# Performance work log

Measured on AMD Instinct MI355X. Metric: run time of the kernel, lower is better.

Reference implementation:

```python
import jax, jax.numpy as jnp
import numpy as np

B, T, F = 16, 2048, 512


def setup_inputs() -> dict:
    key = jax.random.key(0)
    k1, k2, k3 = jax.random.split(key, 3)
    x = jax.random.normal(k1, (B, T, F), dtype=jnp.float32)
    w_aggr = jax.random.normal(k2, (F, 1), dtype=jnp.float32) * 0.02
    b_aggr = jnp.zeros((1,), dtype=jnp.float32)
    # lengths in [T//2, T] to avoid degenerate lengths[0]==0 (torch would div by 0 too)
    seq_len = jax.random.randint(k3, (B,), T // 2, T + 1).astype(jnp.int32)
    return {"x": x, "w_aggr": w_aggr, "b_aggr": b_aggr, "seq_len": seq_len}


def reference(x, w_aggr, b_aggr, seq_len):
    """Valley-detection dynamic segment-mean pooling.

    Faithful to the torch code, but the O(T^2) triangular-mask bmm is
    expressed as the mathematically identical prefix-sum difference:
    bmm(utri[end]-utri[start], v) == cumsum(v)[end] - cumsum(v)[start].
    Output time dim is padded to T (>= dynamic max_counts); padded segment
    rows have start==end==0 -> numerator 0 / clamp -> exactly 0, matching
    the torch zero-padded `valleys` rows.
    """
    Bx, Tx, Fx = x.shape
    wt = jax.nn.sigmoid(x @ w_aggr + b_aggr)[..., 0]          # [B,T] gate weights
    before = jnp.pad(wt[:, :-1], ((0, 0), (1, 0)))            # pad 0 (sigmoid>0 => pos 0 never valley)
    after = jnp.pad(wt[:, 1:], ((0, 0), (0, 1)))              # pad 0 => pos T-1 never valley
    valley = (wt < before) & (wt < after)                     # [B,T] strict local minima
    starts_mask = valley.at[:, 0].set(True)                   # mask[:,0]=True
    ends_mask = valley.at[:, 0].set(False).at[:, -1].set(True)  # mask[:,0]=False; mask[:,-1]=True

    t = jnp.arange(Tx, dtype=jnp.int32)
    bi = jnp.arange(Bx)[:, None]

    def pack(m, vals):
        # left-pack values at True positions into fixed [B,T] (zeros beyond count)
        rank = jnp.cumsum(m, axis=1) - 1
        slot = jnp.where(m, rank, Tx)                         # dump non-selected into slot T
        out = jnp.zeros((Bx, Tx + 1), jnp.int32).at[bi, slot].set(vals)
        return out[:, :Tx], jnp.sum(m, axis=1)

    starts, counts = pack(starts_mask, jnp.broadcast_to(t, (Bx, Tx)))
    end_vals = jnp.broadcast_to(jnp.minimum(t + 2, Tx), (Bx, Tx))  # valley_index_end clipped to length
    ends, _ = pack(ends_mask, end_vals)

    alpha_h = wt[..., None] * x                               # [B,T,F]
    # exclusive->inclusive prefix sums with leading zero row
    cs_ah = jnp.concatenate([jnp.zeros((Bx, 1, Fx), x.dtype), jnp.cumsum(alpha_h, axis=1)], axis=1)
    cs_w = jnp.concatenate([jnp.zeros((Bx, 1), x.dtype), jnp.cumsum(wt, axis=1)], axis=1)

    num = cs_ah[bi, ends] - cs_ah[bi, starts]                 # [B,T,F] segment sums of w*x
    den = jnp.clip(cs_w[bi, ends] - cs_w[bi, starts], 1e-6, None)[..., None]
    pooled = num / den                                        # weighted segment mean

    max_counts = jnp.max(counts)
    lengths = jnp.minimum(seq_len, Tx)
    new_lengths = (lengths.astype(jnp.float32) / lengths[0].astype(jnp.float32)
                   * max_counts.astype(jnp.float32)).astype(jnp.int32)
    new_mask = t[None, :] < new_lengths[:, None]              # [B,T]
    return pooled, new_mask
```

## Files before the change

### kernel.cpp

```cpp
#include <hip/hip_runtime.h>
#include <math.h>

#define BB 16
#define TT 2048
#define FF 512

#define ACTIVE_BLOCKS 8192
#define ZERO_BLOCKS   1024
#define MASK_BLOCKS   32

typedef float v4f __attribute__((ext_vector_type(4)));

__global__ __launch_bounds__(256) void wt_kernel(const float* __restrict__ x,
                                                 const float* __restrict__ w,
                                                 const float* __restrict__ bias,
                                                 float* __restrict__ wt) {
    int gid  = blockIdx.x * 256 + threadIdx.x;
    int row  = gid >> 6;
    int lane = gid & 63;
    const float* xr = x + (size_t)row * FF + lane * 8;
    const float* wr = w + lane * 8;
    float4 a0 = *(const float4*)xr;
    float4 a1 = *(const float4*)(xr + 4);
    float4 w0 = *(const float4*)wr;
    float4 w1 = *(const float4*)(wr + 4);
    float s = a0.x * w0.x + a0.y * w0.y + a0.z * w0.z + a0.w * w0.w
            + a1.x * w1.x + a1.y * w1.y + a1.z * w1.z + a1.w * w1.w;
#pragma unroll
    for (int off = 32; off > 0; off >>= 1) s += __shfl_xor(s, off, 64);
    if (lane == 0) {
        float z = s + bias[0];
        wt[row] = 1.0f / (1.0f + expf(-z));
    }
}

__global__ __launch_bounds__(64) void seg_kernel(const float* __restrict__ wt,
                                                 int* __restrict__ starts,
                                                 int* __restrict__ ends,
                                                 int* __restrict__ counts) {
    int b    = blockIdx.x;
    int lane = threadIdx.x;
    const float* wrow = wt + b * TT;
    float v[32];
    const float4* p = (const float4*)(wrow + lane * 32);
#pragma unroll
    for (int k = 0; k < 8; ++k) {
        float4 f = p[k];
        v[4*k] = f.x; v[4*k+1] = f.y; v[4*k+2] = f.z; v[4*k+3] = f.w;
    }
    float left  = __shfl_up(v[31], 1, 64);
    float right = __shfl_down(v[0], 1, 64);
    unsigned int flags = 0;
#pragma unroll
    for (int k = 0; k < 32; ++k) {
        int t = lane * 32 + k;
        float prev = (k == 0)  ? left  : v[k - 1];
        float next = (k == 31) ? right : v[k + 1];
        bool val = (t > 0) && (t < TT - 1) && (v[k] < prev) && (v[k] < next);
        if (val) flags |= (1u << k);
    }
    int cnt = __popc(flags);
    int inc = cnt;
#pragma unroll
    for (int off = 1; off < 64; off <<= 1) {
        int y = __shfl_up(inc, off, 64);
        if (lane >= off) inc += y;
    }
    int total = __shfl(inc, 63, 64);
    int r = inc - cnt;
    int* sb = starts + b * TT;
    int* eb = ends + b * TT;
    unsigned int f = flags;
    while (f) {
        int k = __ffs(f) - 1;
        f &= f - 1;
        int t = lane * 32 + k;
        sb[r + 1] = t;
        eb[r] = t + 2;
        ++r;
    }
    if (lane == 0) {
        sb[0] = 0;
        eb[total] = TT;
        counts[b] = total + 1;
    }
}

__global__ __launch_bounds__(256) void pool_kernel(const float* __restrict__ x,
                                                   const float* __restrict__ wt,
                                                   const int* __restrict__ starts,
                                                   const int* __restrict__ ends,
                                                   const int* __restrict__ counts,
                                                   const int* __restrict__ seq_len,
                                                   float* __restrict__ out,
                                                   float* __restrict__ mask_out) {
    int blk = blockIdx.x;
    int tid = threadIdx.x;
    v4f zero = (v4f)(0.f);

    if (blk >= ACTIVE_BLOCKS + ZERO_BLOCKS) {
        int idx = (blk - ACTIVE_BLOCKS - ZERO_BLOCKS) * 256 + tid;
        int maxc = 0;
#pragma unroll
        for (int i = 0; i < BB; ++i) maxc = max(maxc, counts[i]);
        float len0 = (float)min(seq_len[0], TT);
#pragma unroll
        for (int r = 0; r < 4; ++r) {
            int i = idx + r * 8192;
            int b = i >> 11, t = i & (TT - 1);
            int nl = (int)((float)min(seq_len[b], TT) / len0 * (float)maxc);
            mask_out[i] = (t < nl) ? 1.0f : 0.0f;
        }
        return;
    }

    if (blk >= ACTIVE_BLOCKS) {
        int zb = blk - ACTIVE_BLOCKS;
        int b  = zb >> 6;
        int j0 = 1024 + (zb & 63) * 16;
        float* base = out + ((size_t)(b * TT + j0) * FF);
        v4f* dst = (v4f*)base + tid * 2;
        __builtin_nontemporal_store(zero, dst);
        __builtin_nontemporal_store(zero, dst + 1);
        return;
    }

    int wv    = tid >> 6;
    int lane  = tid & 63;
    int aw    = blk * 4 + wv;
    int rowid = aw >> 1;
    int half  = aw & 1;
    int b     = rowid >> 10;
    int j     = rowid & 1023;
    int row   = b * TT + j;
    int fo    = half * 256 + lane * 4;

    v4f acc = (v4f)(0.f);
    if (j < counts[b]) {
        int s = __builtin_amdgcn_readfirstlane(starts[row]);
        int e = __builtin_amdgcn_readfirstlane(ends[row]);
        const float* xb   = x + (size_t)b * TT * FF + fo;
        const float* wrow = wt + b * TT;
        float den = 0.f;
        for (int t = s; t < e; t += 8) {
            int   ii[8];
            float ww[8];
#pragma unroll
            for (int k = 0; k < 8; ++k) {
                int tt = t + k;
                bool in = (tt < e);
                ii[k] = in ? tt : t;
                ww[k] = in ? wrow[ii[k]] : 0.f;
            }
#pragma unroll
            for (int k = 0; k < 8; ++k) {
                const v4f* p = (const v4f*)(xb + (size_t)ii[k] * FF);
                v4f v0 = p[0];
                acc += ww[k] * v0;
                den += ww[k];
            }
        }
        acc *= 1.0f / fmaxf(den, 1e-6f);
    }
    float* orow = out + (size_t)row * FF + fo;
    __builtin_nontemporal_store(acc, (v4f*)orow);
}

extern "C" void kernel_launch(void* const* d_in, const int* in_sizes, int n_in,
                              void* d_out, int out_size, void* d_ws, size_t ws_size,
                              hipStream_t stream) {
    const float* x       = (const float*)d_in[0];
    const float* w_aggr  = (const float*)d_in[1];
    const float* b_aggr  = (const float*)d_in[2];
    const int*   seq_len = (const int*)d_in[3];

    float* pooled = (float*)d_out;
    float* mask   = (float*)d_out + (size_t)BB * TT * FF;

    float* wt    = (float*)d_ws;
    int* starts  = (int*)((char*)d_ws + (size_t)BB * TT * 4);
    int* ends    = starts + BB * TT;
    int* counts  = ends + BB * TT;

    wt_kernel<<<(BB * TT) / 4, 256, 0, stream>>>(x, w_aggr, b_aggr, wt);
    seg_kernel<<<BB, 64, 0, stream>>>(wt, starts, ends, counts);
    pool_kernel<<<ACTIVE_BLOCKS + ZERO_BLOCKS + MASK_BLOCKS, 256, 0, stream>>>(
        x, wt, starts, ends, counts, seq_len, pooled, mask);
}
```

Measured before the change: 129.4 us.

## Move zero-fill of padded rows into wt kernel; one wave per pooled row

```diff
diff --git a/kernel.cpp b/kernel.cpp
--- a/kernel.cpp
+++ b/kernel.cpp
@@ -5,17 +5,32 @@
 #define TT 2048
 #define FF 512
 
-#define ACTIVE_BLOCKS 8192
-#define ZERO_BLOCKS   1024
-#define MASK_BLOCKS   32
+#define WT_BLOCKS   8192
+#define ZERO_BLOCKS 1024
+#define ACTIVE_BLOCKS 4096
+#define MASK_BLOCKS 32
 
 typedef float v4f __attribute__((ext_vector_type(4)));
 
-__global__ __launch_bounds__(256) void wt_kernel(const float* __restrict__ x,
-                                                 const float* __restrict__ w,
-                                                 const float* __restrict__ bias,
-                                                 float* __restrict__ wt) {
-    int gid  = blockIdx.x * 256 + threadIdx.x;
+__global__ __launch_bounds__(256) void wt_zero_kernel(const float* __restrict__ x,
+                                                      const float* __restrict__ w,
+                                                      const float* __restrict__ bias,
+                                                      float* __restrict__ wt,
+                                                      float* __restrict__ out) {
+    int blk = blockIdx.x;
+    int tid = threadIdx.x;
+    if (blk >= WT_BLOCKS) {
+        int zb = blk - WT_BLOCKS;
+        int b  = zb >> 6;
+        int j0 = 1024 + (zb & 63) * 16;
+        float* base = out + ((size_t)(b * TT + j0) * FF);
+        v4f zero = (v4f)(0.f);
+        v4f* dst = (v4f*)base + tid * 2;
+        __builtin_nontemporal_store(zero, dst);
+        __builtin_nontemporal_store(zero, dst + 1);
+        return;
+    }
+    int gid  = blk * 256 + tid;
     int row  = gid >> 6;
     int lane = gid & 63;
     const float* xr = x + (size_t)row * FF + lane * 8;
@@ -96,10 +111,9 @@
                                                    float* __restrict__ mask_out) {
     int blk = blockIdx.x;
     int tid = threadIdx.x;
-    v4f zero = (v4f)(0.f);
 
-    if (blk >= ACTIVE_BLOCKS + ZERO_BLOCKS) {
-        int idx = (blk - ACTIVE_BLOCKS - ZERO_BLOCKS) * 256 + tid;
+    if (blk >= ACTIVE_BLOCKS) {
+        int idx = (blk - ACTIVE_BLOCKS) * 256 + tid;
         int maxc = 0;
 #pragma unroll
         for (int i = 0; i < BB; ++i) maxc = max(maxc, counts[i]);
@@ -114,32 +128,19 @@
         return;
     }
 
-    if (blk >= ACTIVE_BLOCKS) {
-        int zb = blk - ACTIVE_BLOCKS;
-        int b  = zb >> 6;
-        int j0 = 1024 + (zb & 63) * 16;
-        float* base = out + ((size_t)(b * TT + j0) * FF);
-        v4f* dst = (v4f*)base + tid * 2;
-        __builtin_nontemporal_store(zero, dst);
-        __builtin_nontemporal_store(zero, dst + 1);
-        return;
-    }
+    int b    = blk >> 8;
+    int wv   = tid >> 6;
+    int lane = tid & 63;
+    int j    = (blk & 255) * 4 + wv;
+    int row  = b * TT + j;
+    float* orow = out + (size_t)row * FF + lane * 8;
 
-    int wv    = tid >> 6;
-    int lane  = tid & 63;
-    int aw    = blk * 4 + wv;
-    int rowid = aw >> 1;
-    int half  = aw & 1;
-    int b     = rowid >> 10;
-    int j     = rowid & 1023;
-    int row   = b * TT + j;
-    int fo    = half * 256 + lane * 4;
-
-    v4f acc = (v4f)(0.f);
+    v4f acc0 = (v4f)(0.f);
+    v4f acc1 = (v4f)(0.f);
     if (j < counts[b]) {
         int s = __builtin_amdgcn_readfirstlane(starts[row]);
         int e = __builtin_amdgcn_readfirstlane(ends[row]);
-        const float* xb   = x + (size_t)b * TT * FF + fo;
+        const float* xb   = x + (size_t)b * TT * FF + lane * 8;
         const float* wrow = wt + b * TT;
         float den = 0.f;
         for (int t = s; t < e; t += 8) {
@@ -155,15 +156,17 @@
 #pragma unroll
             for (int k = 0; k < 8; ++k) {
                 const v4f* p = (const v4f*)(xb + (size_t)ii[k] * FF);
-                v4f v0 = p[0];
-                acc += ww[k] * v0;
-                den += ww[k];
+                v4f v0 = p[0], v1 = p[1];
+                acc0 += ww[k] * v0;
+                acc1 += ww[k] * v1;
+                den  += ww[k];
             }
         }
-        acc *= 1.0f / fmaxf(den, 1e-6f);
+        float inv = 1.0f / fmaxf(den, 1e-6f);
+        acc0 *= inv; acc1 *= inv;
     }
-    float* orow = out + (size_t)row * FF + fo;
-    __builtin_nontemporal_store(acc, (v4f*)orow);
+    __builtin_nontemporal_store(acc0, (v4f*)orow);
+    __builtin_nontemporal_store(acc1, (v4f*)(orow + 4));
 }
 
 extern "C" void kernel_launch(void* const* d_in, const int* in_sizes, int n_in,
@@ -182,8 +185,8 @@
     int* ends    = starts + BB * TT;
     int* counts  = ends + BB * TT;
 
-    wt_kernel<<<(BB * TT) / 4, 256, 0, stream>>>(x, w_aggr, b_aggr, wt);
+    wt_zero_kernel<<<WT_BLOCKS + ZERO_BLOCKS, 256, 0, stream>>>(x, w_aggr, b_aggr, wt, pooled);
     seg_kernel<<<BB, 64, 0, stream>>>(wt, starts, ends, counts);
-    pool_kernel<<<ACTIVE_BLOCKS + ZERO_BLOCKS + MASK_BLOCKS, 256, 0, stream>>>(
+    pool_kernel<<<ACTIVE_BLOCKS + MASK_BLOCKS, 256, 0, stream>>>(
         x, wt, starts, ends, counts, seq_len, pooled, mask);
 }
```

Result: no change. 130.4 us (+0.8%).
